# Kernel tuning notes

Measured on AMD Instinct MI355X. Metric: run time of the kernel, lower is better.

The kernel has to match this reference:

```python
import jax, jax.numpy as jnp
import numpy as np

B, D, E, K, H, C = 8192, 1024, 8, 2, 2048, 512
LN_EPS = 1e-5


def setup_inputs() -> dict:
    key = jax.random.key(0)
    ks = jax.random.split(key, 6)
    s = 0.02
    return {
        "x": jax.random.normal(ks[0], (B, D), dtype=jnp.float32),
        "Wr": jax.random.normal(ks[1], (E, D), dtype=jnp.float32) * s,  # router weight [E,D]
        "br": jnp.zeros((E,), dtype=jnp.float32),
        "gamma": jnp.ones((E, D), dtype=jnp.float32),   # per-expert LayerNorm scale
        "beta": jnp.zeros((E, D), dtype=jnp.float32),   # per-expert LayerNorm shift
        "W1": jax.random.normal(ks[2], (E, H, D), dtype=jnp.float32) * s,
        "b1": jnp.zeros((E, H), dtype=jnp.float32),
        "W2": jax.random.normal(ks[3], (E, C, H), dtype=jnp.float32) * s,
        "b2": jnp.zeros((E, C), dtype=jnp.float32),
    }


def reference(x, Wr, br, gamma, beta, W1, b1, W2, b2):
    # Router + top-k gating (softmax over the k selected logits only)
    router_logits = x @ Wr.T + br                       # [B,E]
    topk_vals, topk_idx = jax.lax.top_k(router_logits, K)  # [B,K]
    topk_w = jax.nn.softmax(topk_vals, axis=-1)         # [B,K]
    # Dense gate [B,E]: gate[b,e] = sum_j topk_w[b,j] * (topk_idx[b,j]==e)
    gate = (jax.nn.one_hot(topk_idx, E, dtype=x.dtype) * topk_w[..., None]).sum(axis=1)

    # LayerNorm statistics are expert-independent; affine is per-expert
    mu = x.mean(axis=-1, keepdims=True)
    var = ((x - mu) ** 2).mean(axis=-1, keepdims=True)
    xn = (x - mu) * jax.lax.rsqrt(var + LN_EPS)          # [B,D]

    out = jnp.zeros((x.shape[0], C), dtype=x.dtype)
    for e in range(E):  # small fixed expert count
        xe = xn * gamma[e] + beta[e]                     # [B,D]
        h = jax.nn.gelu(xe @ W1[e].T + b1[e], approximate=False)  # [B,H]
        y = h @ W2[e].T + b2[e]                          # [B,C]
        out = out + gate[:, e:e + 1] * y
    return out
```

## Files before the change

kernel.cpp:

```cpp
#include <hip/hip_runtime.h>
#include <hip/hip_bf16.h>
#include <math.h>

#define B_TOK 8192
#define DDIM 1024
#define NEXP 8
#define HDIM 2048
#define CDIM 512
#define LN_EPS 1e-5f
#define MAXT256 72
#define MAXROWS (MAXT256 * 256)

typedef __attribute__((ext_vector_type(4))) float f32x4;
typedef __attribute__((ext_vector_type(8))) short bf16x8;

__device__ __forceinline__ unsigned short f2bf(float f) {
  __hip_bfloat16 h = __float2bfloat16(f);
  return *reinterpret_cast<unsigned short*>(&h);
}
__device__ __forceinline__ float bf2f(unsigned short u) {
  unsigned int x = ((unsigned int)u) << 16;
  return *reinterpret_cast<float*>(&x);
}

__device__ __forceinline__ void gload_lds16(const unsigned short* g, unsigned short* l) {
  __builtin_amdgcn_global_load_lds(
      (const __attribute__((address_space(1))) unsigned int*)g,
      (__attribute__((address_space(3))) unsigned int*)l, 16, 0, 0);
}

__global__ __launch_bounds__(256) void router_ln_kernel(
    const float* __restrict__ x, const float* __restrict__ Wr,
    const float* __restrict__ br, int* __restrict__ eidx,
    float* __restrict__ wgt, unsigned short* __restrict__ xn) {
  const int wid = threadIdx.x >> 6;
  const int lane = threadIdx.x & 63;
  const int tok = blockIdx.x * 4 + wid;

  const float4* xr = reinterpret_cast<const float4*>(x + (size_t)tok * DDIM);
  float4 xv[4];
  float sum = 0.f, sumsq = 0.f;
  float dot[NEXP];
#pragma unroll
  for (int e = 0; e < NEXP; ++e) dot[e] = 0.f;

#pragma unroll
  for (int i = 0; i < 4; ++i) {
    const int f = i * 64 + lane;
    float4 v = xr[f];
    xv[i] = v;
    sum += v.x + v.y + v.z + v.w;
    sumsq += v.x * v.x + v.y * v.y + v.z * v.z + v.w * v.w;
#pragma unroll
    for (int e = 0; e < NEXP; ++e) {
      float4 w = reinterpret_cast<const float4*>(Wr + e * DDIM)[f];
      dot[e] += v.x * w.x + v.y * w.y + v.z * w.z + v.w * w.w;
    }
  }
#pragma unroll
  for (int off = 32; off > 0; off >>= 1) {
    sum += __shfl_xor(sum, off);
    sumsq += __shfl_xor(sumsq, off);
#pragma unroll
    for (int e = 0; e < NEXP; ++e) dot[e] += __shfl_xor(dot[e], off);
  }
  const float mu = sum * (1.f / DDIM);
  const float var = sumsq * (1.f / DDIM) - mu * mu;
  const float rs = rsqrtf(var + LN_EPS);

  float lg[NEXP];
#pragma unroll
  for (int e = 0; e < NEXP; ++e) lg[e] = dot[e] + br[e];

  int i1 = 0; float v1 = lg[0];
#pragma unroll
  for (int e = 1; e < NEXP; ++e) { if (lg[e] > v1) { v1 = lg[e]; i1 = e; } }
  int i2 = -1; float v2 = -3.4e38f;
#pragma unroll
  for (int e = 0; e < NEXP; ++e) { if (e != i1 && lg[e] > v2) { v2 = lg[e]; i2 = e; } }

  const float e2 = __expf(v2 - v1);
  const float inv = 1.f / (1.f + e2);
  if (lane == 0) {
    eidx[tok * 2] = i1; eidx[tok * 2 + 1] = i2;
    wgt[tok * 2] = inv; wgt[tok * 2 + 1] = e2 * inv;
  }

  unsigned short* xnr = xn + (size_t)tok * DDIM;
#pragma unroll
  for (int i = 0; i < 4; ++i) {
    const int f = i * 64 + lane;
    float4 v = xv[i];
    ushort4 o;
    o.x = f2bf((v.x - mu) * rs);
    o.y = f2bf((v.y - mu) * rs);
    o.z = f2bf((v.z - mu) * rs);
    o.w = f2bf((v.w - mu) * rs);
    reinterpret_cast<ushort4*>(xnr)[f] = o;
  }
}

__global__ __launch_bounds__(256) void sort_kernel(
    const int* __restrict__ eidx,
    int* __restrict__ tokRow,
    int* __restrict__ slot2row,
    int* __restrict__ tileExp,
    int* __restrict__ nTilesOut) {
  __shared__ int cnt[NEXP], segBase[NEXP], cur[NEXP];
  const int tid = threadIdx.x;
  if (tid < NEXP) { cnt[tid] = 0; cur[tid] = 0; }
  __syncthreads();
  for (int t = tid; t < B_TOK * 2; t += 256)
    atomicAdd(&cnt[eidx[t]], 1);
  __syncthreads();
  if (tid == 0) {
    int c = 0;
    for (int e = 0; e < NEXP; ++e) {
      segBase[e] = c;
      const int nt = (cnt[e] + 255) >> 8;
      for (int t = 0; t < nt; ++t) tileExp[(c >> 8) + t] = e;
      for (int p = c + cnt[e]; p < c + nt * 256; ++p) tokRow[p] = 0;
      c += nt * 256;
    }
    *nTilesOut = c >> 8;
  }
  __syncthreads();
  for (int t = tid; t < B_TOK * 2; t += 256) {
    const int e = eidx[t];
    const int pos = segBase[e] + atomicAdd(&cur[e], 1);
    tokRow[pos] = t >> 1;
    slot2row[t] = pos;
  }
}

__global__ __launch_bounds__(256) void prep_w1_kernel(
    const float* __restrict__ W1, const float* __restrict__ gamma,
    const float* __restrict__ beta, const float* __restrict__ b1,
    unsigned short* __restrict__ W1g, float* __restrict__ c1) {
  const int eh = blockIdx.x;
  const int e = eh >> 11;
  const int tid = threadIdx.x;

  float4 w = reinterpret_cast<const float4*>(W1 + (size_t)eh * DDIM)[tid];
  float4 g = reinterpret_cast<const float4*>(gamma + (size_t)e * DDIM)[tid];
  float4 bt = reinterpret_cast<const float4*>(beta + (size_t)e * DDIM)[tid];

  ushort4 o;
  o.x = f2bf(w.x * g.x); o.y = f2bf(w.y * g.y);
  o.z = f2bf(w.z * g.z); o.w = f2bf(w.w * g.w);
  reinterpret_cast<ushort4*>(W1g + (size_t)eh * DDIM)[tid] = o;

  float p = w.x * bt.x + w.y * bt.y + w.z * bt.z + w.w * bt.w;
#pragma unroll
  for (int off = 32; off > 0; off >>= 1) p += __shfl_xor(p, off);
  __shared__ float red[4];
  const int lane = tid & 63, wv = tid >> 6;
  if (lane == 0) red[wv] = p;
  __syncthreads();
  if (tid == 0) c1[eh] = b1[eh] + red[0] + red[1] + red[2] + red[3];
}

__global__ __launch_bounds__(256) void prep_w2_kernel(
    const float* __restrict__ W2, unsigned short* __restrict__ W2b) {
  const int idx = blockIdx.x * 256 + threadIdx.x;
  float4 w = reinterpret_cast<const float4*>(W2)[idx];
  ushort4 o;
  o.x = f2bf(w.x); o.y = f2bf(w.y); o.z = f2bf(w.z); o.w = f2bf(w.w);
  reinterpret_cast<ushort4*>(W2b)[idx] = o;
}

template <int KS>
__device__ __forceinline__ void phase32(
    const unsigned short* ldsA, const unsigned short* ldsB,
    int wm, int wn, int l15, int l4, f32x4 (&acc)[8][4]) {
  bf16x8 af[8], bfr[4];
  const int slot = ((KS * 4 + l4) ^ (l15 & 7)) * 8;
#pragma unroll
  for (int mm = 0; mm < 8; ++mm)
    af[mm] = *reinterpret_cast<const bf16x8*>(
        &ldsA[(wm * 128 + mm * 16 + l15) * 64 + slot]);
#pragma unroll
  for (int nn = 0; nn < 4; ++nn)
    bfr[nn] = *reinterpret_cast<const bf16x8*>(
        &ldsB[(wn * 64 + nn * 16 + l15) * 64 + slot]);
  asm volatile("s_barrier" ::: "memory");
  __builtin_amdgcn_s_setprio(1);
#pragma unroll
  for (int mm = 0; mm < 8; ++mm)
#pragma unroll
    for (int nn = 0; nn < 4; ++nn)
      acc[mm][nn] = __builtin_amdgcn_mfma_f32_16x16x32_bf16(af[mm], bfr[nn], acc[mm][nn], 0, 0, 0);
  __builtin_amdgcn_s_setprio(0);
  asm volatile("s_barrier" ::: "memory");
}

__global__ __launch_bounds__(512, 2) void gemm1_8p_kernel(
    const unsigned short* __restrict__ A,
    const unsigned short* __restrict__ W1g,
    const float* __restrict__ c1,
    const int* __restrict__ tokRow, const int* __restrict__ tileExp,
    const int* __restrict__ nTiles,
    unsigned short* __restrict__ Hout) {
  const int bx = blockIdx.x, by = blockIdx.y;
  if (bx >= *nTiles) return;
  const int e = tileExp[bx];

  __shared__ unsigned short lds[2][2][256 * 64];

  const int tid = threadIdx.x;
  const int lane = tid & 63;
  const int wid = tid >> 6;
  const int wm = wid >> 2;
  const int wn = wid & 3;
  const int l15 = lane & 15, l4 = lane >> 4;

  const unsigned short* Bg = W1g + ((size_t)e * HDIM + (size_t)by * 256) * DDIM;

  int tr[4];
#pragma unroll
  for (int i = 0; i < 4; ++i) tr[i] = tokRow[bx * 256 + i * 64 + (tid >> 3)];
  const int sl8 = ((tid & 7) ^ ((tid >> 3) & 7)) * 8;

  f32x4 acc[8][4];
#pragma unroll
  for (int m = 0; m < 8; ++m)
#pragma unroll
    for (int n = 0; n < 4; ++n)
#pragma unroll
      for (int j = 0; j < 4; ++j) acc[m][n][j] = 0.f;

  auto stage8 = [&](int b, int k0) {
#pragma unroll
    for (int h = 0; h < 2; ++h)
#pragma unroll
      for (int q = 0; q < 2; ++q)
        gload_lds16(A + (size_t)tr[h * 2 + q] * DDIM + k0 + sl8,
                    &lds[b][0][h * 8192 + q * 4096 + tid * 8]);
#pragma unroll
    for (int h = 0; h < 2; ++h)
#pragma unroll
      for (int q = 0; q < 2; ++q)
        gload_lds16(Bg + (size_t)(h * 128 + q * 64 + (tid >> 3)) * DDIM + k0 + sl8,
                    &lds[b][1][h * 8192 + q * 4096 + tid * 8]);
  };

  stage8(0, 0);
  stage8(1, 64);

  int cur = 0;
#pragma unroll 1
  for (int kt = 0; kt < 15; ++kt) {
    asm volatile("s_waitcnt vmcnt(8)" ::: "memory");
    __builtin_amdgcn_sched_barrier(0);
    asm volatile("s_barrier" ::: "memory");
    const unsigned short* ldsA = lds[cur][0];
    const unsigned short* ldsB = lds[cur][1];
    phase32<0>(ldsA, ldsB, wm, wn, l15, l4, acc);
    phase32<1>(ldsA, ldsB, wm, wn, l15, l4, acc);
    if (kt < 14) stage8(cur, (kt + 2) * 64);
    cur ^= 1;
  }
  asm volatile("s_waitcnt vmcnt(0)" ::: "memory");
  __builtin_amdgcn_sched_barrier(0);
  asm volatile("s_barrier" ::: "memory");
  {
    const unsigned short* ldsA = lds[cur][0];
    const unsigned short* ldsB = lds[cur][1];
    phase32<0>(ldsA, ldsB, wm, wn, l15, l4, acc);
    phase32<1>(ldsA, ldsB, wm, wn, l15, l4, acc);
  }

  const float* biasp = c1 + e * HDIM + by * 256 + wn * 64;
  unsigned short* Hbase = Hout + (size_t)(bx * 256 + wm * 128) * HDIM + by * 256 + wn * 64;
#pragma unroll
  for (int m = 0; m < 8; ++m) {
#pragma unroll
    for (int n = 0; n < 4; ++n) {
      const int col = n * 16 + l15;
      const float bv = biasp[col];
#pragma unroll
      for (int j = 0; j < 4; ++j) {
        const int row = m * 16 + l4 * 4 + j;
        const float v = acc[m][n][j] + bv;
        const float gl = 0.5f * v * (1.f + erff(v * 0.70710678118654752f));
        Hbase[(size_t)row * HDIM + col] = f2bf(gl);
      }
    }
  }
}

#define BM 128
#define BN 128
#define BKK 64

__global__ __launch_bounds__(256) void gemm2_kernel(
    const unsigned short* __restrict__ Hbuf,
    const unsigned short* __restrict__ W2b,
    const int* __restrict__ tileExp, const int* __restrict__ nTiles,
    unsigned short* __restrict__ Y) {
  const int bx = blockIdx.x, by = blockIdx.y;
  if ((bx >> 1) >= *nTiles) return;
  const int e = tileExp[bx >> 1];

  __shared__ unsigned short lA[BM * BKK];
  __shared__ unsigned short lB[BN * BKK];
  const int tid = threadIdx.x;
  const int lane = tid & 63;
  const int wid = tid >> 6;
  const int wr = wid >> 1, wc = wid & 1;

  const unsigned short* Abase = Hbuf + (size_t)bx * BM * HDIM;
  const unsigned short* Bbase = W2b + ((size_t)e * CDIM + (size_t)by * BN) * HDIM;

  f32x4 acc[4][4];
#pragma unroll
  for (int m = 0; m < 4; ++m)
#pragma unroll
    for (int n = 0; n < 4; ++n)
#pragma unroll
      for (int j = 0; j < 4; ++j) acc[m][n][j] = 0.f;

  const int r = tid >> 3;
  const int cc = (tid & 7) * 8;

  for (int k0 = 0; k0 < HDIM; k0 += BKK) {
#pragma unroll
    for (int i = 0; i < 4; ++i)
      gload_lds16(Abase + (size_t)(i * 32 + r) * HDIM + k0 + cc,
                  &lA[(i * 32 + r) * BKK + cc]);
#pragma unroll
    for (int i = 0; i < 4; ++i)
      gload_lds16(Bbase + (size_t)(i * 32 + r) * HDIM + k0 + cc,
                  &lB[(i * 32 + r) * BKK + cc]);
    __syncthreads();
#pragma unroll
    for (int kk = 0; kk < 2; ++kk) {
      bf16x8 af[4], bfr[4];
      const int kof = kk * 32 + (lane >> 4) * 8;
#pragma unroll
      for (int m = 0; m < 4; ++m)
        af[m] = *reinterpret_cast<const bf16x8*>(
            &lA[(wr * 64 + m * 16 + (lane & 15)) * BKK + kof]);
#pragma unroll
      for (int n = 0; n < 4; ++n)
        bfr[n] = *reinterpret_cast<const bf16x8*>(
            &lB[(wc * 64 + n * 16 + (lane & 15)) * BKK + kof]);
#pragma unroll
      for (int m = 0; m < 4; ++m)
#pragma unroll
        for (int n = 0; n < 4; ++n)
          acc[m][n] = __builtin_amdgcn_mfma_f32_16x16x32_bf16(af[m], bfr[n], acc[m][n], 0, 0, 0);
    }
    __syncthreads();
  }

  const int row0 = bx * BM + wr * 64;
  const int col0 = by * BN + wc * 64;
#pragma unroll
  for (int m = 0; m < 4; ++m) {
#pragma unroll
    for (int j = 0; j < 4; ++j) {
      const int row = row0 + m * 16 + (lane >> 4) * 4 + j;
#pragma unroll
      for (int n = 0; n < 4; ++n) {
        const int col = col0 + n * 16 + (lane & 15);
        Y[(size_t)row * CDIM + col] = f2bf(acc[m][n][j]);
      }
    }
  }
}

__global__ __launch_bounds__(256) void combine_kernel(
    const unsigned short* __restrict__ Y, const int* __restrict__ slot2row,
    const int* __restrict__ eidx, const float* __restrict__ wgt,
    const float* __restrict__ b2, float* __restrict__ out) {
  const int idx = blockIdx.x * 256 + threadIdx.x;
  const int b = idx >> 7;
  const int c4 = (idx & 127) * 4;
  const int r0 = slot2row[b * 2], r1 = slot2row[b * 2 + 1];
  const int e0 = eidx[b * 2], e1 = eidx[b * 2 + 1];
  const float w0 = wgt[b * 2], w1 = wgt[b * 2 + 1];
  ushort4 y0 = *reinterpret_cast<const ushort4*>(Y + (size_t)r0 * CDIM + c4);
  ushort4 y1 = *reinterpret_cast<const ushort4*>(Y + (size_t)r1 * CDIM + c4);
  float4 bb0 = *reinterpret_cast<const float4*>(b2 + e0 * CDIM + c4);
  float4 bb1 = *reinterpret_cast<const float4*>(b2 + e1 * CDIM + c4);
  float4 o;
  o.x = w0 * (bf2f(y0.x) + bb0.x) + w1 * (bf2f(y1.x) + bb1.x);
  o.y = w0 * (bf2f(y0.y) + bb0.y) + w1 * (bf2f(y1.y) + bb1.y);
  o.z = w0 * (bf2f(y0.z) + bb0.z) + w1 * (bf2f(y1.z) + bb1.z);
  o.w = w0 * (bf2f(y0.w) + bb0.w) + w1 * (bf2f(y1.w) + bb1.w);
  *reinterpret_cast<float4*>(out + (size_t)b * CDIM + c4) = o;
}

extern "C" void kernel_launch(void* const* d_in, const int* in_sizes, int n_in,
                              void* d_out, int out_size, void* d_ws, size_t ws_size,
                              hipStream_t stream) {
  const float* x     = (const float*)d_in[0];
  const float* Wr    = (const float*)d_in[1];
  const float* br    = (const float*)d_in[2];
  const float* gamma = (const float*)d_in[3];
  const float* beta  = (const float*)d_in[4];
  const float* W1    = (const float*)d_in[5];
  const float* b1    = (const float*)d_in[6];
  const float* W2    = (const float*)d_in[7];
  const float* b2    = (const float*)d_in[8];
  float* out = (float*)d_out;

  char* ws = (char*)d_ws;
  unsigned short* xn   = (unsigned short*)(ws);
  unsigned short* W2b  = (unsigned short*)(ws);
  unsigned short* hbuf = (unsigned short*)(ws + (size_t)16 * 1048576);
  unsigned short* W1g  = (unsigned short*)(ws + (size_t)88 * 1048576);
  unsigned short* ybuf = (unsigned short*)(ws + (size_t)88 * 1048576);
  char* misc           = ws + (size_t)120 * 1048576;
  float* c1      = (float*)(misc);
  int* eidx      = (int*)(misc + 65536);
  float* wgt     = (float*)(misc + 2 * 65536);
  int* slot2row  = (int*)(misc + 3 * 65536);
  int* tokRow    = (int*)(misc + 4 * 65536);
  int* tileExp   = (int*)(misc + 4 * 65536 + 131072);
  int* nTiles    = tileExp + MAXT256;

  router_ln_kernel<<<dim3(B_TOK / 4), dim3(256), 0, stream>>>(x, Wr, br, eidx, wgt, xn);
  sort_kernel<<<dim3(1), dim3(256), 0, stream>>>(eidx, tokRow, slot2row, tileExp, nTiles);
  prep_w1_kernel<<<dim3(NEXP * HDIM), dim3(256), 0, stream>>>(W1, gamma, beta, b1, W1g, c1);

  gemm1_8p_kernel<<<dim3(MAXT256, HDIM / 256), dim3(512), 0, stream>>>(
      xn, W1g, c1, tokRow, tileExp, nTiles, hbuf);

  prep_w2_kernel<<<dim3((NEXP * CDIM * HDIM / 4) / 256), dim3(256), 0, stream>>>(W2, W2b);

  gemm2_kernel<<<dim3(MAXT256 * 2, CDIM / BN), dim3(256), 0, stream>>>(
      hbuf, W2b, tileExp, nTiles, ybuf);
  combine_kernel<<<dim3(B_TOK * CDIM / 4 / 256), dim3(256), 0, stream>>>(
      ybuf, slot2row, eidx, wgt, b2, out);
}
```

Measured before the change: 308.6 us.

## Deepen gemm1 to a 4-stage BK=32 pipeline and remap block order for both GEMMs

The first expert GEMM drops its double-buffered BK=64 loop and uses a 4-buffer ring of BK=32 tiles. Loads run three tiles ahead and are issued after the LDS fragment reads, so each step needs one barrier fewer. Launch bounds drop to one block per CU, and the grid is flattened so the eight N-blocks of one token tile run next to each other, which aims for better L2 reuse of the A rows. gemm2 also gets a flattened grid with an interleaved block remap for locality. The risks are lower occupancy, more loop iterations, and correctness of the waitcnt accounting in the new pipeline.

New measurement: 315.2 us. +2.1%, slower.

```diff
diff --git a/kernel.cpp b/kernel.cpp
--- a/kernel.cpp
+++ b/kernel.cpp
@@ -169,43 +169,20 @@
   reinterpret_cast<ushort4*>(W2b)[idx] = o;
 }
 
-template <int KS>
-__device__ __forceinline__ void phase32(
-    const unsigned short* ldsA, const unsigned short* ldsB,
-    int wm, int wn, int l15, int l4, f32x4 (&acc)[8][4]) {
-  bf16x8 af[8], bfr[4];
-  const int slot = ((KS * 4 + l4) ^ (l15 & 7)) * 8;
-#pragma unroll
-  for (int mm = 0; mm < 8; ++mm)
-    af[mm] = *reinterpret_cast<const bf16x8*>(
-        &ldsA[(wm * 128 + mm * 16 + l15) * 64 + slot]);
-#pragma unroll
-  for (int nn = 0; nn < 4; ++nn)
-    bfr[nn] = *reinterpret_cast<const bf16x8*>(
-        &ldsB[(wn * 64 + nn * 16 + l15) * 64 + slot]);
-  asm volatile("s_barrier" ::: "memory");
-  __builtin_amdgcn_s_setprio(1);
-#pragma unroll
-  for (int mm = 0; mm < 8; ++mm)
-#pragma unroll
-    for (int nn = 0; nn < 4; ++nn)
-      acc[mm][nn] = __builtin_amdgcn_mfma_f32_16x16x32_bf16(af[mm], bfr[nn], acc[mm][nn], 0, 0, 0);
-  __builtin_amdgcn_s_setprio(0);
-  asm volatile("s_barrier" ::: "memory");
-}
-
-__global__ __launch_bounds__(512, 2) void gemm1_8p_kernel(
+__global__ __launch_bounds__(512, 1) void gemm1_pipe_kernel(
     const unsigned short* __restrict__ A,
     const unsigned short* __restrict__ W1g,
     const float* __restrict__ c1,
     const int* __restrict__ tokRow, const int* __restrict__ tileExp,
     const int* __restrict__ nTiles,
     unsigned short* __restrict__ Hout) {
-  const int bx = blockIdx.x, by = blockIdx.y;
+  const int bid = blockIdx.x;
+  const int by = bid & 7;
+  const int bx = bid >> 3;
   if (bx >= *nTiles) return;
   const int e = tileExp[bx];
 
-  __shared__ unsigned short lds[2][2][256 * 64];
+  __shared__ unsigned short lds[4][2][256 * 32];
 
   const int tid = threadIdx.x;
   const int lane = tid & 63;
@@ -216,10 +193,11 @@
 
   const unsigned short* Bg = W1g + ((size_t)e * HDIM + (size_t)by * 256) * DDIM;
 
-  int tr[4];
-#pragma unroll
-  for (int i = 0; i < 4; ++i) tr[i] = tokRow[bx * 256 + i * 64 + (tid >> 3)];
-  const int sl8 = ((tid & 7) ^ ((tid >> 3) & 7)) * 8;
+  const int srow = tid >> 2;
+  const int sg8 = (((tid & 3) ^ (srow & 3))) * 8;
+  int tr2[2];
+#pragma unroll
+  for (int j = 0; j < 2; ++j) tr2[j] = tokRow[bx * 256 + j * 128 + srow];
 
   f32x4 acc[8][4];
 #pragma unroll
@@ -229,46 +207,61 @@
 #pragma unroll
       for (int j = 0; j < 4; ++j) acc[m][n][j] = 0.f;
 
-  auto stage8 = [&](int b, int k0) {
-#pragma unroll
-    for (int h = 0; h < 2; ++h)
-#pragma unroll
-      for (int q = 0; q < 2; ++q)
-        gload_lds16(A + (size_t)tr[h * 2 + q] * DDIM + k0 + sl8,
-                    &lds[b][0][h * 8192 + q * 4096 + tid * 8]);
-#pragma unroll
-    for (int h = 0; h < 2; ++h)
-#pragma unroll
-      for (int q = 0; q < 2; ++q)
-        gload_lds16(Bg + (size_t)(h * 128 + q * 64 + (tid >> 3)) * DDIM + k0 + sl8,
-                    &lds[b][1][h * 8192 + q * 4096 + tid * 8]);
+  auto stage = [&](int buf, int k0) {
+#pragma unroll
+    for (int j = 0; j < 2; ++j)
+      gload_lds16(A + (size_t)tr2[j] * DDIM + k0 + sg8,
+                  &lds[buf][0][j * 4096 + tid * 8]);
+#pragma unroll
+    for (int j = 0; j < 2; ++j)
+      gload_lds16(Bg + (size_t)(j * 128 + srow) * DDIM + k0 + sg8,
+                  &lds[buf][1][j * 4096 + tid * 8]);
   };
 
-  stage8(0, 0);
-  stage8(1, 64);
-
-  int cur = 0;
+  const int rslot = (l4 ^ (l15 & 3)) * 8;
+
+  auto do_tile = [&](int buf, int kt, bool stageNext) {
+    const unsigned short* la = &lds[buf][0][0];
+    const unsigned short* lb = &lds[buf][1][0];
+    bf16x8 af[8], bfr[4];
+#pragma unroll
+    for (int mm = 0; mm < 8; ++mm)
+      af[mm] = *reinterpret_cast<const bf16x8*>(
+          &la[(wm * 128 + mm * 16 + l15) * 32 + rslot]);
+#pragma unroll
+    for (int nn = 0; nn < 4; ++nn)
+      bfr[nn] = *reinterpret_cast<const bf16x8*>(
+          &lb[(wn * 64 + nn * 16 + l15) * 32 + rslot]);
+    if (stageNext) stage((kt + 3) & 3, (kt + 3) * 32);
+    asm volatile("s_barrier" ::: "memory");
+    __builtin_amdgcn_s_setprio(1);
+#pragma unroll
+    for (int mm = 0; mm < 8; ++mm)
+#pragma unroll
+      for (int nn = 0; nn < 4; ++nn)
+        acc[mm][nn] = __builtin_amdgcn_mfma_f32_16x16x32_bf16(af[mm], bfr[nn], acc[mm][nn], 0, 0, 0);
+    __builtin_amdgcn_s_setprio(0);
+  };
+
+  stage(0, 0);
+  stage(1, 32);
+  stage(2, 64);
+
 #pragma unroll 1
-  for (int kt = 0; kt < 15; ++kt) {
+  for (int kt = 0; kt < 30; ++kt) {
     asm volatile("s_waitcnt vmcnt(8)" ::: "memory");
     __builtin_amdgcn_sched_barrier(0);
     asm volatile("s_barrier" ::: "memory");
-    const unsigned short* ldsA = lds[cur][0];
-    const unsigned short* ldsB = lds[cur][1];
-    phase32<0>(ldsA, ldsB, wm, wn, l15, l4, acc);
-    phase32<1>(ldsA, ldsB, wm, wn, l15, l4, acc);
-    if (kt < 14) stage8(cur, (kt + 2) * 64);
-    cur ^= 1;
-  }
+    do_tile(kt & 3, kt, kt < 29);
+  }
+  asm volatile("s_waitcnt vmcnt(4)" ::: "memory");
+  __builtin_amdgcn_sched_barrier(0);
+  asm volatile("s_barrier" ::: "memory");
+  do_tile(30 & 3, 30, false);
   asm volatile("s_waitcnt vmcnt(0)" ::: "memory");
   __builtin_amdgcn_sched_barrier(0);
   asm volatile("s_barrier" ::: "memory");
-  {
-    const unsigned short* ldsA = lds[cur][0];
-    const unsigned short* ldsB = lds[cur][1];
-    phase32<0>(ldsA, ldsB, wm, wn, l15, l4, acc);
-    phase32<1>(ldsA, ldsB, wm, wn, l15, l4, acc);
-  }
+  do_tile(31 & 3, 31, false);
 
   const float* biasp = c1 + e * HDIM + by * 256 + wn * 64;
   unsigned short* Hbase = Hout + (size_t)(bx * 256 + wm * 128) * HDIM + by * 256 + wn * 64;
@@ -298,7 +291,10 @@
     const unsigned short* __restrict__ W2b,
     const int* __restrict__ tileExp, const int* __restrict__ nTiles,
     unsigned short* __restrict__ Y) {
-  const int bx = blockIdx.x, by = blockIdx.y;
+  const int flat = blockIdx.x;
+  const int virt = (flat & 7) * 72 + (flat >> 3);
+  const int bx = virt % 144;
+  const int by = virt / 144;
   if ((bx >> 1) >= *nTiles) return;
   const int e = tileExp[bx >> 1];
 
@@ -425,12 +421,12 @@
   sort_kernel<<<dim3(1), dim3(256), 0, stream>>>(eidx, tokRow, slot2row, tileExp, nTiles);
   prep_w1_kernel<<<dim3(NEXP * HDIM), dim3(256), 0, stream>>>(W1, gamma, beta, b1, W1g, c1);
 
-  gemm1_8p_kernel<<<dim3(MAXT256, HDIM / 256), dim3(512), 0, stream>>>(
+  gemm1_pipe_kernel<<<dim3(MAXT256 * 8), dim3(512), 0, stream>>>(
       xn, W1g, c1, tokRow, tileExp, nTiles, hbuf);
 
   prep_w2_kernel<<<dim3((NEXP * CDIM * HDIM / 4) / 256), dim3(256), 0, stream>>>(W2, W2b);
 
-  gemm2_kernel<<<dim3(MAXT256 * 2, CDIM / BN), dim3(256), 0, stream>>>(
+  gemm2_kernel<<<dim3(MAXT256 * 2 * (CDIM / BN)), dim3(256), 0, stream>>>(
       hbuf, W2b, tileExp, nTiles, ybuf);
   combine_kernel<<<dim3(B_TOK * CDIM / 4 / 256), dim3(256), 0, stream>>>(
       ybuf, slot2row, eidx, wgt, b2, out);
```
